# Performance work log

Measured on AMD Instinct MI355X. Metric: run time of the kernel, lower is better.

Reference implementation:

```python
import jax, jax.numpy as jnp
import numpy as np

C, H, W = 256, 50, 50       # backbone feature map (stride-16, 800px image)
N_BOXES = 512
P = 7                       # output_size
SCALE = 1.0 / 16.0          # spatial_scale
IMG = 800.0


def setup_inputs() -> dict:
    key = jax.random.key(0)
    k1, k2, k3 = jax.random.split(key, 3)
    feature_map = jax.random.normal(k1, (1, C, H, W), dtype=jnp.float32)
    xy = jax.random.uniform(k2, (N_BOXES, 2), jnp.float32, 0.0, IMG * 0.75)
    wh = jax.random.uniform(k3, (N_BOXES, 2), jnp.float32, 16.0, IMG * 0.25)
    x2y2 = jnp.minimum(xy + wh, IMG - 1.0)
    bboxes = jnp.concatenate([xy, x2y2], axis=1)  # [N,4] (x1,y1,x2,y2)
    return {"feature_map": feature_map, "bboxes": bboxes,
            "output_size": P, "spatial_scale": SCALE}


def _roi_pool(feat, boxes, pooled, scale):
    # feat: [1,C,H,W]; boxes: [N,4]. Faithful to torchvision roi_pool (all boxes on image 0).
    f = feat[0]                                   # [C,H,W]
    Ch, Hh, Ww = f.shape
    # round-half-away-from-zero like C roundf (coords are non-negative)
    r = jnp.floor(boxes * scale + 0.5).astype(jnp.int32)
    x1, y1, x2, y2 = r[:, 0], r[:, 1], r[:, 2], r[:, 3]
    rw = jnp.maximum(x2 - x1 + 1, 1)              # roi_width  [N]
    rh = jnp.maximum(y2 - y1 + 1, 1)              # roi_height [N]
    pb = jnp.arange(pooled, dtype=jnp.int32)
    # bin boundaries (exact integer floor/ceil division), clamped to feature extent
    hs = jnp.clip((pb[None, :] * rh[:, None]) // pooled + y1[:, None], 0, Hh)          # [N,P]
    he = jnp.clip(((pb[None, :] + 1) * rh[:, None] + pooled - 1) // pooled + y1[:, None], 0, Hh)
    ws = jnp.clip((pb[None, :] * rw[:, None]) // pooled + x1[:, None], 0, Ww)
    we = jnp.clip(((pb[None, :] + 1) * rw[:, None] + pooled - 1) // pooled + x1[:, None], 0, Ww)
    hidx = jnp.arange(Hh, dtype=jnp.int32)
    widx = jnp.arange(Ww, dtype=jnp.int32)
    mh = (hidx[None, None, :] >= hs[..., None]) & (hidx[None, None, :] < he[..., None])  # [N,P,H]
    mw = (widx[None, None, :] >= ws[..., None]) & (widx[None, None, :] < we[..., None])  # [N,P,W]
    NEG = jnp.float32(-jnp.inf)
    # stage 1: masked max over rows for each ph bin -> [N,P,C,W]
    rows = jnp.stack(
        [jnp.max(jnp.where(mh[:, p, None, :, None], f[None], NEG), axis=2) for p in range(pooled)],
        axis=1)
    # stage 2: masked max over cols for each pw bin -> [N,Ph,Pw,C]
    out = jnp.stack(
        [jnp.max(jnp.where(mw[:, q, None, None, :], rows, NEG), axis=3) for q in range(pooled)],
        axis=2)
    out = jnp.transpose(out, (0, 3, 1, 2))        # [N,C,Ph,Pw]
    empty = (he <= hs)[:, :, None] | (we <= ws)[:, None, :]  # [N,Ph,Pw]
    return jnp.where(empty[:, None, :, :], jnp.float32(0.0), out)


def reference(feature_map, bboxes, output_size, spatial_scale):
    return _roi_pool(feature_map, bboxes, int(output_size), spatial_scale)
```

## Files before the change

kernel.cpp:

```cpp
#include <hip/hip_runtime.h>


#define CC   256
#define HH   50
#define WW   50
#define NBOX 512
#define PP   7
#define SCL  (1.0f / 16.0f)
#define HW   (HH * WW)
#define OUT_PER_BOX (CC * PP * PP)

__global__ __launch_bounds__(256) void transpose_kernel(
    const float* __restrict__ feat, float* __restrict__ featT)
{
    __shared__ float tile[64][65];
    int tc = blockIdx.x & 3;
    int th = blockIdx.x >> 2;
    int c0 = tc * 64, h0 = th * 64;
    int lane = threadIdx.x & 63;
    int row4 = threadIdx.x >> 6;

    for (int it = 0; it < 16; ++it) {
        int r  = row4 + it * 4;
        int hw = h0 + lane;
        if (hw < HW)
            tile[r][lane] = feat[(c0 + r) * HW + hw];
    }
    __syncthreads();
    for (int it = 0; it < 16; ++it) {
        int r  = row4 + it * 4;
        int hw = h0 + r;
        if (hw < HW)
            featT[hw * CC + c0 + lane] = tile[lane][r];
    }
}

__global__ __launch_bounds__(512) void pool_kernel(
    const float* __restrict__ featT,
    const float* __restrict__ boxes,
    float* __restrict__ out)
{
    __shared__ float res[OUT_PER_BOX];
    int n    = blockIdx.x;
    int tid  = threadIdx.x;
    int wave = tid >> 6;
    int lane = tid & 63;

    const float* b = boxes + n * 4;
    int x1 = (int)floorf(b[0] * SCL + 0.5f);
    int y1 = (int)floorf(b[1] * SCL + 0.5f);
    int x2 = (int)floorf(b[2] * SCL + 0.5f);
    int y2 = (int)floorf(b[3] * SCL + 0.5f);
    int rw = max(x2 - x1 + 1, 1);
    int rh = max(y2 - y1 + 1, 1);

    for (int pq = wave; pq < PP * PP; pq += 8) {
        int p = pq / PP, q = pq % PP;
        int hs = min(max(p * rh / PP + y1, 0), HH);
        int he = min(max(((p + 1) * rh + PP - 1) / PP + y1, 0), HH);
        int ws = min(max(q * rw / PP + x1, 0), WW);
        int we = min(max(((q + 1) * rw + PP - 1) / PP + x1, 0), WW);

        float m0 = -INFINITY, m1 = m0, m2 = m0, m3 = m0;
        for (int h = hs; h < he; ++h) {
            const float* base = featT + h * (WW * CC) + lane;
            for (int w = ws; w < we; ++w) {
                const float* pc = base + w * CC;
                m0 = fmaxf(m0, pc[0]);
                m1 = fmaxf(m1, pc[64]);
                m2 = fmaxf(m2, pc[128]);
                m3 = fmaxf(m3, pc[192]);
            }
        }
        if ((he <= hs) || (we <= ws)) { m0 = m1 = m2 = m3 = 0.0f; }

        res[(lane      ) * 49 + pq] = m0;
        res[(lane +  64) * 49 + pq] = m1;
        res[(lane + 128) * 49 + pq] = m2;
        res[(lane + 192) * 49 + pq] = m3;
    }
    __syncthreads();

    const float4* r4 = (const float4*)res;
    float4*       o4 = (float4*)(out + n * OUT_PER_BOX);
    for (int i = tid; i < OUT_PER_BOX / 4; i += 512)
        o4[i] = r4[i];
}

__global__ __launch_bounds__(256) void pool_direct_kernel(
    const float* __restrict__ feat,
    const float* __restrict__ boxes,
    float* __restrict__ out, int total)
{
    int idx = blockIdx.x * blockDim.x + threadIdx.x;
    if (idx >= total) return;
    int q = idx % PP;
    int t = idx / PP;
    int p = t % PP;
    t /= PP;
    int c = t & (CC - 1);
    int n = t >> 8;

    const float* b = boxes + n * 4;
    int x1 = (int)floorf(b[0] * SCL + 0.5f);
    int y1 = (int)floorf(b[1] * SCL + 0.5f);
    int x2 = (int)floorf(b[2] * SCL + 0.5f);
    int y2 = (int)floorf(b[3] * SCL + 0.5f);
    int rw = max(x2 - x1 + 1, 1);
    int rh = max(y2 - y1 + 1, 1);

    int hs = min(max(p * rh / PP + y1, 0), HH);
    int he = min(max(((p + 1) * rh + PP - 1) / PP + y1, 0), HH);
    int ws = min(max(q * rw / PP + x1, 0), WW);
    int we = min(max(((q + 1) * rw + PP - 1) / PP + x1, 0), WW);

    const float* fc = feat + c * HW;
    float m = -INFINITY;
    for (int h = hs; h < he; ++h)
        for (int w = ws; w < we; ++w)
            m = fmaxf(m, fc[h * WW + w]);
    out[idx] = ((he <= hs) || (we <= ws)) ? 0.0f : m;
}

extern "C" void kernel_launch(void* const* d_in, const int* in_sizes, int n_in,
                              void* d_out, int out_size, void* d_ws, size_t ws_size,
                              hipStream_t stream)
{
    const float* feat  = (const float*)d_in[0];
    const float* boxes = (const float*)d_in[1];
    float* out = (float*)d_out;

    const size_t needT = (size_t)HW * CC * sizeof(float);
    if (ws_size >= needT) {
        float* featT = (float*)d_ws;
        transpose_kernel<<<40 * 4, 256, 0, stream>>>(feat, featT);
        pool_kernel<<<NBOX, 512, 0, stream>>>(featT, boxes, out);
    } else {
        int total = NBOX * CC * PP * PP;
        pool_direct_kernel<<<(total + 255) / 256, 256, 0, stream>>>(
            feat, boxes, out, total);
    }
}
```

Before: 27.40 us.

## Fuse transpose and pooling into one cooperative kernel with float4 gathers

Merges the transpose kernel and the pooling kernel into a single cooperative launch. The first 160 blocks transpose the feature map, a grid-wide sync follows, then every block pools one RoI. The goal is to remove one kernel launch and the gap between the two kernels. The pooling loop now loads a float4 per lane (4 consecutive channels) instead of four strided scalars, and the final write un-permutes channels from shared memory with scalar stores. In exchange, the grid barrier adds cost, and the cooperative launch needs all 512 blocks of 512 threads resident at once (512 blocks, about 49KB LDS each), otherwise the launch can fail.

```diff
diff --git a/kernel.cpp b/kernel.cpp
--- a/kernel.cpp
+++ b/kernel.cpp
@@ -1,4 +1,7 @@
 #include <hip/hip_runtime.h>
+#include <hip/hip_cooperative_groups.h>
+
+namespace cg = cooperative_groups;
 
 
 #define CC   256
@@ -9,42 +12,44 @@
 #define SCL  (1.0f / 16.0f)
 #define HW   (HH * WW)
 #define OUT_PER_BOX (CC * PP * PP)
+#define NBIN (PP * PP)
 
-__global__ __launch_bounds__(256) void transpose_kernel(
-    const float* __restrict__ feat, float* __restrict__ featT)
+__global__ __launch_bounds__(512) void fused_roipool_kernel(
+    const float* __restrict__ feat,
+    const float* __restrict__ boxes,
+    float* __restrict__ out,
+    float* __restrict__ featT)
 {
-    __shared__ float tile[64][65];
-    int tc = blockIdx.x & 3;
-    int th = blockIdx.x >> 2;
-    int c0 = tc * 64, h0 = th * 64;
-    int lane = threadIdx.x & 63;
-    int row4 = threadIdx.x >> 6;
+    __shared__ float smem[OUT_PER_BOX];
+    int bid  = blockIdx.x;
+    int tid  = threadIdx.x;
+    int lane = tid & 63;
 
-    for (int it = 0; it < 16; ++it) {
-        int r  = row4 + it * 4;
-        int hw = h0 + lane;
-        if (hw < HW)
-            tile[r][lane] = feat[(c0 + r) * HW + hw];
+    if (bid < 160) {
+        float (*tile)[65] = (float(*)[65])smem;
+        int tc = bid & 3;
+        int th = bid >> 2;
+        int c0 = tc * 64, h0 = th * 64;
+        int r8 = tid >> 6;
+        for (int it = 0; it < 8; ++it) {
+            int r  = r8 + it * 8;
+            int hw = h0 + lane;
+            if (hw < HW)
+                tile[r][lane] = feat[(c0 + r) * HW + hw];
+        }
+        __syncthreads();
+        for (int it = 0; it < 8; ++it) {
+            int r  = r8 + it * 8;
+            int hw = h0 + r;
+            if (hw < HW)
+                featT[hw * CC + c0 + lane] = tile[lane][r];
+        }
     }
-    __syncthreads();
-    for (int it = 0; it < 16; ++it) {
-        int r  = row4 + it * 4;
-        int hw = h0 + r;
-        if (hw < HW)
-            featT[hw * CC + c0 + lane] = tile[lane][r];
-    }
-}
 
-__global__ __launch_bounds__(512) void pool_kernel(
-    const float* __restrict__ featT,
-    const float* __restrict__ boxes,
-    float* __restrict__ out)
-{
-    __shared__ float res[OUT_PER_BOX];
-    int n    = blockIdx.x;
-    int tid  = threadIdx.x;
+    cg::this_grid().sync();
+
+    int n    = bid;
     int wave = tid >> 6;
-    int lane = tid & 63;
 
     const float* b = boxes + n * 4;
     int x1 = (int)floorf(b[0] * SCL + 0.5f);
@@ -54,37 +59,42 @@
     int rw = max(x2 - x1 + 1, 1);
     int rh = max(y2 - y1 + 1, 1);
 
-    for (int pq = wave; pq < PP * PP; pq += 8) {
+    const float* fl = featT + 4 * lane;
+
+    for (int pq = wave; pq < NBIN; pq += 8) {
         int p = pq / PP, q = pq % PP;
         int hs = min(max(p * rh / PP + y1, 0), HH);
         int he = min(max(((p + 1) * rh + PP - 1) / PP + y1, 0), HH);
         int ws = min(max(q * rw / PP + x1, 0), WW);
         int we = min(max(((q + 1) * rw + PP - 1) / PP + x1, 0), WW);
 
-        float m0 = -INFINITY, m1 = m0, m2 = m0, m3 = m0;
+        float4 m = make_float4(-INFINITY, -INFINITY, -INFINITY, -INFINITY);
         for (int h = hs; h < he; ++h) {
-            const float* base = featT + h * (WW * CC) + lane;
+            const float* base = fl + h * (WW * CC);
             for (int w = ws; w < we; ++w) {
-                const float* pc = base + w * CC;
-                m0 = fmaxf(m0, pc[0]);
-                m1 = fmaxf(m1, pc[64]);
-                m2 = fmaxf(m2, pc[128]);
-                m3 = fmaxf(m3, pc[192]);
+                float4 v = *(const float4*)(base + w * CC);
+                m.x = fmaxf(m.x, v.x);
+                m.y = fmaxf(m.y, v.y);
+                m.z = fmaxf(m.z, v.z);
+                m.w = fmaxf(m.w, v.w);
             }
         }
-        if ((he <= hs) || (we <= ws)) { m0 = m1 = m2 = m3 = 0.0f; }
+        if ((he <= hs) || (we <= ws))
+            m = make_float4(0.0f, 0.0f, 0.0f, 0.0f);
 
-        res[(lane      ) * 49 + pq] = m0;
-        res[(lane +  64) * 49 + pq] = m1;
-        res[(lane + 128) * 49 + pq] = m2;
-        res[(lane + 192) * 49 + pq] = m3;
+        int base = lane * 49 + pq;
+        smem[base           ] = m.x;
+        smem[base + 1 * 3136] = m.y;
+        smem[base + 2 * 3136] = m.z;
+        smem[base + 3 * 3136] = m.w;
     }
     __syncthreads();
 
-    const float4* r4 = (const float4*)res;
-    float4*       o4 = (float4*)(out + n * OUT_PER_BOX);
-    for (int i = tid; i < OUT_PER_BOX / 4; i += 512)
-        o4[i] = r4[i];
+    float* on = out + n * OUT_PER_BOX;
+    for (int i = tid; i < OUT_PER_BOX; i += 512) {
+        int c = i / 49, pq = i % 49;
+        on[i] = smem[((c & 3) * 64 + (c >> 2)) * 49 + pq];
+    }
 }
 
 __global__ __launch_bounds__(256) void pool_direct_kernel(
@@ -133,8 +143,9 @@
     const size_t needT = (size_t)HW * CC * sizeof(float);
     if (ws_size >= needT) {
         float* featT = (float*)d_ws;
-        transpose_kernel<<<40 * 4, 256, 0, stream>>>(feat, featT);
-        pool_kernel<<<NBOX, 512, 0, stream>>>(featT, boxes, out);
+        void* args[] = { (void*)&feat, (void*)&boxes, (void*)&out, (void*)&featT };
+        hipLaunchCooperativeKernel((const void*)fused_roipool_kernel,
+                                   dim3(NBOX), dim3(512), args, 0, stream);
     } else {
         int total = NBOX * CC * PP * PP;
         pool_direct_kernel<<<(total + 255) / 256, 256, 0, stream>>>(
```

Result: slower. 97.87 us (+257.2%).
